# Performance work log

Measured on AMD Instinct MI355X. Metric: run time of the kernel, lower is better.

The kernel has to match this reference:

```python
import jax, jax.numpy as jnp
import numpy as np

B, N, F, C = 8, 4096, 1024, 64


def setup_inputs() -> dict:
    key = jax.random.key(0)
    k1, k2, k3 = jax.random.split(key, 3)
    x1 = jax.random.normal(k1, (B, N, F), dtype=jnp.float32)
    x2 = jax.random.normal(k2, (B, N, F), dtype=jnp.float32)
    W = jax.random.normal(k3, (C, F), dtype=jnp.float32) / np.sqrt(F)
    b = jnp.zeros((C,), dtype=jnp.float32)
    return {"x1": x1, "x2": x2, "W": W, "b": b}


def _select_max(x, W, b):
    # x: [B, N, F] -> scores [B, N, C]
    scores = jnp.einsum("bnf,cf->bnc", x, W) + b
    # per-batch, per-class index of max-scoring instance: [B, C]
    idx = jnp.argmax(scores, axis=1)
    # gather the selected instance feature vectors: [B, C, F]
    return jnp.take_along_axis(x, idx[:, :, None], axis=1)


def reference(x1, x2, W, b):
    d = _select_max(x1, W, b)
    d1 = _select_max(x2, W, b)
    return (d, d1)
```

## Files before the change

### kernel.cpp

```cpp
#include <hip/hip_runtime.h>

#define B_   8
#define N_   4096
#define F_   1024
#define C_   64
#define NBLK 16
#define MARGIN 0.08f

typedef __attribute__((ext_vector_type(8))) short bhalf8;
typedef __attribute__((ext_vector_type(4))) float f32x4;
typedef __attribute__((ext_vector_type(4))) unsigned short us4;

__device__ __forceinline__ unsigned short f2bf_rne(float x) {
    unsigned u = __builtin_bit_cast(unsigned, x);
    u += 0x7fffu + ((u >> 16) & 1u);
    return (unsigned short)(u >> 16);
}
__device__ __forceinline__ bhalf8 cvt8(float4 a, float4 b) {
    bhalf8 r;
    r[0] = (short)f2bf_rne(a.x); r[1] = (short)f2bf_rne(a.y);
    r[2] = (short)f2bf_rne(a.z); r[3] = (short)f2bf_rne(a.w);
    r[4] = (short)f2bf_rne(b.x); r[5] = (short)f2bf_rne(b.y);
    r[6] = (short)f2bf_rne(b.z); r[7] = (short)f2bf_rne(b.w);
    return r;
}

#define LEXGT(a, ai, b, bi) ((a) > (b) || ((a) == (b) && (ai) < (bi)))
#define INSERT3(vv, nn)                                                        \
    do {                                                                       \
        float _v = (vv); int _n = (nn);                                        \
        if (LEXGT(_v, _n, v0, i0)) { v2=v1; i2=i1; v1=v0; i1=i0; v0=_v; i0=_n; } \
        else if (LEXGT(_v, _n, v1, i1)) { v2=v1; i2=i1; v1=_v; i1=_n; }        \
        else if (LEXGT(_v, _n, v2, i2)) { v2=_v; i2=_n; }                      \
    } while (0)
#define INSERT4(vv, nn)                                                        \
    do {                                                                       \
        float _v = (vv); int _n = (nn);                                        \
        if (LEXGT(_v, _n, v0, i0)) { v3=v2; i3=i2; v2=v1; i2=i1; v1=v0; i1=i0; v0=_v; i0=_n; } \
        else if (LEXGT(_v, _n, v1, i1)) { v3=v2; i3=i2; v2=v1; i2=i1; v1=_v; i1=_n; } \
        else if (LEXGT(_v, _n, v2, i2)) { v3=v2; i3=i2; v2=_v; i2=_n; }        \
        else if (LEXGT(_v, _n, v3, i3)) { v3=_v; i3=_n; }                      \
    } while (0)

__global__ __launch_bounds__(256) void wconv_kernel(
    const float* __restrict__ W, unsigned short* __restrict__ Wh)
{
    int i = blockIdx.x * 256 + threadIdx.x;
    float4 v = ((const float4*)W)[i];
    us4 hh;
    hh[0] = f2bf_rne(v.x); hh[1] = f2bf_rne(v.y);
    hh[2] = f2bf_rne(v.z); hh[3] = f2bf_rne(v.w);
    ((us4*)Wh)[i] = hh;
}

__global__ __launch_bounds__(1024, 4) void score_top_kernel(
    const float* __restrict__ x1, const float* __restrict__ x2,
    const unsigned short* __restrict__ Wh,
    float* __restrict__ pv, int* __restrict__ pi)
{
    __shared__ __align__(16) char lds[131072];

    const int tid  = threadIdx.x;
    const int nb   = blockIdx.x;
    const int b    = blockIdx.y;
    const int inp  = blockIdx.z;
    const float* __restrict__ x = inp ? x2 : x1;

    const int lane = tid & 63;
    const int w    = tid >> 6;
    const int rsel = lane & 15;
    const int g    = lane >> 4;
    const int swz  = (rsel & 7) << 4;

    const int row = nb * 256 + w * 16 + rsel;
    const float* __restrict__ xr = x + ((size_t)b * N_ + row) * F_ + g * 8;

    f32x4 acc[4];
    #pragma unroll
    for (int nt = 0; nt < 4; ++nt) acc[nt] = (f32x4){0.f, 0.f, 0.f, 0.f};

    auto loadx = [&](float4* dst, int kc) {
        #pragma unroll
        for (int st = 0; st < 4; ++st) {
            dst[2 * st]     = *(const float4*)(xr + kc * 128 + st * 32);
            dst[2 * st + 1] = *(const float4*)(xr + kc * 128 + st * 32 + 4);
        }
    };
    auto compute = [&](const float4* src, int kc) {
        #pragma unroll
        for (int st = 0; st < 4; ++st) {
            bhalf8 ah = cvt8(src[2 * st], src[2 * st + 1]);
            int kb = kc * 256 + st * 64 + g * 16;
            #pragma unroll
            for (int nt = 0; nt < 4; ++nt) {
                int cls = nt * 16 + rsel;
                bhalf8 bf = *(const bhalf8*)(lds + ((cls * 2048 + kb) ^ swz));
                acc[nt] = __builtin_amdgcn_mfma_f32_16x16x32_bf16(ah, bf, acc[nt], 0, 0, 0);
            }
        }
    };

    float4 xa[8], xb[8];
    loadx(xa, 0);

    #pragma unroll
    for (int j = 0; j < 8; ++j) {
        int gi = tid + 1024 * j;
        int c = gi >> 7, kq = gi & 127;
        bhalf8 v = *(const bhalf8*)(Wh + (size_t)c * F_ + kq * 8);
        *(bhalf8*)(lds + ((c * 2048 + kq * 16) ^ ((c & 7) << 4))) = v;
    }
    __syncthreads();

    #pragma unroll
    for (int kc = 0; kc < 8; kc += 2) {
        loadx(xb, kc + 1);
        compute(xa, kc);
        if (kc + 2 < 8) loadx(xa, kc + 2);
        compute(xb, kc + 1);
    }

    float wv0[4], wv1[4], wv2[4]; int wi0[4], wi1[4], wi2[4];
    #pragma unroll
    for (int nt = 0; nt < 4; ++nt) {
        float v0 = -3.4e38f, v1 = -3.4e38f, v2 = -3.4e38f;
        int   i0 = 0x7fffffff, i1 = 0x7fffffff, i2 = 0x7fffffff;
        #pragma unroll
        for (int r = 0; r < 4; ++r) {
            int n = nb * 256 + w * 16 + 4 * g + r;
            INSERT3(acc[nt][r], n);
        }
        #pragma unroll
        for (int d = 16; d <= 32; d <<= 1) {
            float u0 = __shfl_xor(v0, d), u1 = __shfl_xor(v1, d), u2 = __shfl_xor(v2, d);
            int   j0 = __shfl_xor(i0, d), j1 = __shfl_xor(i1, d), j2 = __shfl_xor(i2, d);
            INSERT3(u0, j0); INSERT3(u1, j1); INSERT3(u2, j2);
        }
        wv0[nt] = v0; wv1[nt] = v1; wv2[nt] = v2;
        wi0[nt] = i0; wi1[nt] = i1; wi2[nt] = i2;
    }

    __syncthreads();
    float* tv = (float*)lds;
    int*   ti = (int*)(lds + 16384);
    if (lane < 16) {
        #pragma unroll
        for (int nt = 0; nt < 4; ++nt) {
            int c = nt * 16 + lane;
            tv[(w * C_ + c) * 3 + 0] = wv0[nt]; ti[(w * C_ + c) * 3 + 0] = wi0[nt];
            tv[(w * C_ + c) * 3 + 1] = wv1[nt]; ti[(w * C_ + c) * 3 + 1] = wi1[nt];
            tv[(w * C_ + c) * 3 + 2] = wv2[nt]; ti[(w * C_ + c) * 3 + 2] = wi2[nt];
        }
    }
    __syncthreads();

    if (tid < C_) {
        int c = tid;
        float v0 = -3.4e38f, v1 = -3.4e38f, v2 = -3.4e38f, v3 = -3.4e38f;
        int   i0 = 0x7fffffff, i1 = 0x7fffffff, i2 = 0x7fffffff, i3 = 0x7fffffff;
        #pragma unroll 4
        for (int ww = 0; ww < 16; ++ww)
            #pragma unroll
            for (int k = 0; k < 3; ++k)
                INSERT4(tv[(ww * C_ + c) * 3 + k], ti[(ww * C_ + c) * 3 + k]);
        int blk = ((inp * B_ + b) * NBLK + nb);
        pv[(blk * C_ + c) * 4 + 0] = v0; pi[(blk * C_ + c) * 4 + 0] = i0;
        pv[(blk * C_ + c) * 4 + 1] = v1; pi[(blk * C_ + c) * 4 + 1] = i1;
        pv[(blk * C_ + c) * 4 + 2] = v2; pi[(blk * C_ + c) * 4 + 2] = i2;
        pv[(blk * C_ + c) * 4 + 3] = v3; pi[(blk * C_ + c) * 4 + 3] = i3;
    }
}

__global__ __launch_bounds__(256) void select_gather_kernel(
    const float* __restrict__ x1, const float* __restrict__ x2,
    const float* __restrict__ W,
    const float* __restrict__ pv, const int* __restrict__ pi,
    float* __restrict__ out)
{
    const int c   = blockIdx.x;
    const int b   = blockIdx.y;
    const int inp = blockIdx.z;
    const int tid = threadIdx.x;

    __shared__ int   s_cnt;
    __shared__ float s_m;
    __shared__ int   s_cand[16];
    __shared__ float s_val[16];
    __shared__ float s_wsum[4];
    __shared__ int   s_win;

    if (tid == 0) s_cnt = 0;
    __syncthreads();

    if (tid < 64) {
        int nb = tid >> 2, k = tid & 3;
        int blk = ((inp * B_ + b) * NBLK + nb);
        int myoff = (blk * C_ + c) * 4 + k;
        float v = pv[myoff];
        float m = v;
        #pragma unroll
        for (int d = 32; d; d >>= 1) m = fmaxf(m, __shfl_xor(m, d));
        if (tid == 0) s_m = m;
        if (v >= m - MARGIN) {
            int p = atomicAdd(&s_cnt, 1);
            if (p < 16) s_cand[p] = pi[myoff];
        }
    }
    __syncthreads();

    const float* __restrict__ x = inp ? x2 : x1;
    const int ncand = min(s_cnt, 16);
    int winner;
    if (ncand == 1) {
        winner = s_cand[0];
    } else {
        for (int k = 0; k < ncand; ++k) {
            int n = s_cand[k];
            float4 xv = *(const float4*)(x + ((size_t)b * N_ + n) * F_ + tid * 4);
            float4 wq = *(const float4*)(W + (size_t)c * F_ + tid * 4);
            float p = xv.x * wq.x + xv.y * wq.y + xv.z * wq.z + xv.w * wq.w;
            #pragma unroll
            for (int d = 32; d; d >>= 1) p += __shfl_down(p, d);
            if ((tid & 63) == 0) s_wsum[tid >> 6] = p;
            __syncthreads();
            if (tid == 0) s_val[k] = s_wsum[0] + s_wsum[1] + s_wsum[2] + s_wsum[3];
            __syncthreads();
        }
        if (tid == 0) {
            float bv = s_val[0]; int bn = s_cand[0];
            for (int k = 1; k < ncand; ++k)
                if (s_val[k] > bv || (s_val[k] == bv && s_cand[k] < bn)) { bv = s_val[k]; bn = s_cand[k]; }
            s_win = bn;
        }
        __syncthreads();
        winner = s_win;
    }

    float4 vv = *(const float4*)(x + ((size_t)b * N_ + winner) * F_ + tid * 4);
    *(float4*)(out + (((size_t)inp * B_ + b) * C_ + c) * F_ + tid * 4) = vv;
}

extern "C" void kernel_launch(void* const* d_in, const int* in_sizes, int n_in,
                              void* d_out, int out_size, void* d_ws, size_t ws_size,
                              hipStream_t stream) {
    const float* x1 = (const float*)d_in[0];
    const float* x2 = (const float*)d_in[1];
    const float* W  = (const float*)d_in[2];

    unsigned short* Wh = (unsigned short*)d_ws;
    float* pv = (float*)((char*)d_ws + (size_t)C_ * F_ * sizeof(unsigned short));
    int*   pi = (int*)((char*)pv + (size_t)2 * B_ * NBLK * C_ * 4 * sizeof(float));

    wconv_kernel<<<C_ * F_ / 1024, 256, 0, stream>>>(W, Wh);
    dim3 g1(NBLK, B_, 2);
    score_top_kernel<<<g1, 1024, 0, stream>>>(x1, x2, Wh, pv, pi);
    dim3 g2(C_, B_, 2);
    select_gather_kernel<<<g2, 256, 0, stream>>>(x1, x2, W, pv, pi, (float*)d_out);
}
```

Before: 72.49 us.

## Stream x and W tiles through double-buffered LDS with direct global-to-LDS loads

Replaces the per-thread register prefetch of x plus a one-time full W copy into 128KB of LDS with a double-buffered K loop. Each step moves a 32-wide feature chunk of x and the bf16 W into swizzled LDS using global_load_lds. Blocks shrink to 64 rows and 256 threads, so the grid has 1024 blocks and LDS per block is far smaller, which should raise occupancy and overlap the streaming of x. In exchange W is reloaded once per block, every K step needs a barrier, and the candidate lists per block drop from top-4 to top-3, with select_gather adapted to 192 candidates.

```diff
diff --git a/kernel.cpp b/kernel.cpp
--- a/kernel.cpp
+++ b/kernel.cpp
@@ -4,7 +4,10 @@
 #define N_   4096
 #define F_   1024
 #define C_   64
-#define NBLK 16
+#define ROWS 64
+#define KC   32
+#define NT   (F_ / KC)
+#define NBLK (N_ / ROWS)
 #define MARGIN 0.08f
 
 typedef __attribute__((ext_vector_type(8))) short bhalf8;
@@ -24,6 +27,11 @@
     r[6] = (short)f2bf_rne(b.z); r[7] = (short)f2bf_rne(b.w);
     return r;
 }
+__device__ __forceinline__ void load_lds16(const void* g, void* l) {
+    __builtin_amdgcn_global_load_lds(
+        (const __attribute__((address_space(1))) unsigned int*)g,
+        (__attribute__((address_space(3))) unsigned int*)l, 16, 0, 0);
+}
 
 #define LEXGT(a, ai, b, bi) ((a) > (b) || ((a) == (b) && (ai) < (bi)))
 #define INSERT3(vv, nn)                                                        \
@@ -32,14 +40,6 @@
         if (LEXGT(_v, _n, v0, i0)) { v2=v1; i2=i1; v1=v0; i1=i0; v0=_v; i0=_n; } \
         else if (LEXGT(_v, _n, v1, i1)) { v2=v1; i2=i1; v1=_v; i1=_n; }        \
         else if (LEXGT(_v, _n, v2, i2)) { v2=_v; i2=_n; }                      \
-    } while (0)
-#define INSERT4(vv, nn)                                                        \
-    do {                                                                       \
-        float _v = (vv); int _n = (nn);                                        \
-        if (LEXGT(_v, _n, v0, i0)) { v3=v2; i3=i2; v2=v1; i2=i1; v1=v0; i1=i0; v0=_v; i0=_n; } \
-        else if (LEXGT(_v, _n, v1, i1)) { v3=v2; i3=i2; v2=v1; i2=i1; v1=_v; i1=_n; } \
-        else if (LEXGT(_v, _n, v2, i2)) { v3=v2; i3=i2; v2=_v; i2=_n; }        \
-        else if (LEXGT(_v, _n, v3, i3)) { v3=_v; i3=_n; }                      \
     } while (0)
 
 __global__ __launch_bounds__(256) void wconv_kernel(
@@ -53,71 +53,74 @@
     ((us4*)Wh)[i] = hh;
 }
 
-__global__ __launch_bounds__(1024, 4) void score_top_kernel(
+__global__ __launch_bounds__(256, 4) void score_top_kernel(
     const float* __restrict__ x1, const float* __restrict__ x2,
     const unsigned short* __restrict__ Wh,
     float* __restrict__ pv, int* __restrict__ pi)
 {
-    __shared__ __align__(16) char lds[131072];
+    __shared__ __align__(16) char lds[24576];
 
     const int tid  = threadIdx.x;
     const int nb   = blockIdx.x;
     const int b    = blockIdx.y;
     const int inp  = blockIdx.z;
     const float* __restrict__ x = inp ? x2 : x1;
+    const float* __restrict__ xbase = x + ((size_t)b * N_ + (size_t)nb * ROWS) * F_;
 
     const int lane = tid & 63;
     const int w    = tid >> 6;
     const int rsel = lane & 15;
     const int g    = lane >> 4;
-    const int swz  = (rsel & 7) << 4;
-
-    const int row = nb * 256 + w * 16 + rsel;
-    const float* __restrict__ xr = x + ((size_t)b * N_ + row) * F_ + g * 8;
+
+#define XOFF(buf) ((buf) * 8192)
+#define WOFF(buf) (16384 + (buf) * 4096)
+
+#define STAGE(t, buf)                                                          \
+    do {                                                                       \
+        const int f0_ = (t) * KC;                                              \
+        _Pragma("unroll")                                                      \
+        for (int j = 0; j < 2; ++j) {                                          \
+            int ii = w * 2 + j;                                                \
+            int r  = ii * 8 + (lane >> 3);                                     \
+            int cg = (lane & 7) ^ (r & 7);                                     \
+            load_lds16(xbase + (size_t)r * F_ + f0_ + cg * 4,                  \
+                       lds + XOFF(buf) + ii * 1024);                           \
+        }                                                                      \
+        {                                                                      \
+            int cls = w * 16 + (lane >> 2);                                    \
+            int cg  = (lane & 3) ^ ((cls >> 1) & 3);                           \
+            load_lds16(Wh + (size_t)cls * F_ + f0_ + cg * 8,                   \
+                       lds + WOFF(buf) + w * 1024);                            \
+        }                                                                      \
+    } while (0)
 
     f32x4 acc[4];
     #pragma unroll
     for (int nt = 0; nt < 4; ++nt) acc[nt] = (f32x4){0.f, 0.f, 0.f, 0.f};
 
-    auto loadx = [&](float4* dst, int kc) {
-        #pragma unroll
-        for (int st = 0; st < 4; ++st) {
-            dst[2 * st]     = *(const float4*)(xr + kc * 128 + st * 32);
-            dst[2 * st + 1] = *(const float4*)(xr + kc * 128 + st * 32 + 4);
-        }
-    };
-    auto compute = [&](const float4* src, int kc) {
-        #pragma unroll
-        for (int st = 0; st < 4; ++st) {
-            bhalf8 ah = cvt8(src[2 * st], src[2 * st + 1]);
-            int kb = kc * 256 + st * 64 + g * 16;
-            #pragma unroll
-            for (int nt = 0; nt < 4; ++nt) {
-                int cls = nt * 16 + rsel;
-                bhalf8 bf = *(const bhalf8*)(lds + ((cls * 2048 + kb) ^ swz));
-                acc[nt] = __builtin_amdgcn_mfma_f32_16x16x32_bf16(ah, bf, acc[nt], 0, 0, 0);
-            }
-        }
-    };
-
-    float4 xa[8], xb[8];
-    loadx(xa, 0);
-
-    #pragma unroll
-    for (int j = 0; j < 8; ++j) {
-        int gi = tid + 1024 * j;
-        int c = gi >> 7, kq = gi & 127;
-        bhalf8 v = *(const bhalf8*)(Wh + (size_t)c * F_ + kq * 8);
-        *(bhalf8*)(lds + ((c * 2048 + kq * 16) ^ ((c & 7) << 4))) = v;
-    }
-    __syncthreads();
-
-    #pragma unroll
-    for (int kc = 0; kc < 8; kc += 2) {
-        loadx(xb, kc + 1);
-        compute(xa, kc);
-        if (kc + 2 < 8) loadx(xa, kc + 2);
-        compute(xb, kc + 1);
+    const int r_    = w * 16 + rsel;
+    const int aswz0 = ((2 * g)     ^ (r_ & 7)) * 16;
+    const int aswz1 = ((2 * g + 1) ^ (r_ & 7)) * 16;
+
+    STAGE(0, 0);
+    __syncthreads();
+
+    for (int t = 0; t < NT; ++t) {
+        const int cur = t & 1;
+        if (t + 1 < NT) STAGE(t + 1, cur ^ 1);
+
+        const char* xb = lds + XOFF(cur);
+        const char* wb = lds + WOFF(cur);
+        float4 xlo = *(const float4*)(xb + r_ * 128 + aswz0);
+        float4 xhi = *(const float4*)(xb + r_ * 128 + aswz1);
+        bhalf8 ah = cvt8(xlo, xhi);
+        #pragma unroll
+        for (int nt = 0; nt < 4; ++nt) {
+            int cls = nt * 16 + rsel;
+            bhalf8 bf = *(const bhalf8*)(wb + cls * 64 + ((g ^ ((cls >> 1) & 3)) * 16));
+            acc[nt] = __builtin_amdgcn_mfma_f32_16x16x32_bf16(ah, bf, acc[nt], 0, 0, 0);
+        }
+        __syncthreads();
     }
 
     float wv0[4], wv1[4], wv2[4]; int wi0[4], wi1[4], wi2[4];
@@ -127,7 +130,7 @@
         int   i0 = 0x7fffffff, i1 = 0x7fffffff, i2 = 0x7fffffff;
         #pragma unroll
         for (int r = 0; r < 4; ++r) {
-            int n = nb * 256 + w * 16 + 4 * g + r;
+            int n = nb * ROWS + w * 16 + 4 * g + r;
             INSERT3(acc[nt][r], n);
         }
         #pragma unroll
@@ -142,7 +145,7 @@
 
     __syncthreads();
     float* tv = (float*)lds;
-    int*   ti = (int*)(lds + 16384);
+    int*   ti = (int*)(lds + 8192);
     if (lane < 16) {
         #pragma unroll
         for (int nt = 0; nt < 4; ++nt) {
@@ -156,18 +159,17 @@
 
     if (tid < C_) {
         int c = tid;
-        float v0 = -3.4e38f, v1 = -3.4e38f, v2 = -3.4e38f, v3 = -3.4e38f;
-        int   i0 = 0x7fffffff, i1 = 0x7fffffff, i2 = 0x7fffffff, i3 = 0x7fffffff;
-        #pragma unroll 4
-        for (int ww = 0; ww < 16; ++ww)
+        float v0 = -3.4e38f, v1 = -3.4e38f, v2 = -3.4e38f;
+        int   i0 = 0x7fffffff, i1 = 0x7fffffff, i2 = 0x7fffffff;
+        #pragma unroll
+        for (int ww = 0; ww < 4; ++ww)
             #pragma unroll
             for (int k = 0; k < 3; ++k)
-                INSERT4(tv[(ww * C_ + c) * 3 + k], ti[(ww * C_ + c) * 3 + k]);
+                INSERT3(tv[(ww * C_ + c) * 3 + k], ti[(ww * C_ + c) * 3 + k]);
         int blk = ((inp * B_ + b) * NBLK + nb);
-        pv[(blk * C_ + c) * 4 + 0] = v0; pi[(blk * C_ + c) * 4 + 0] = i0;
-        pv[(blk * C_ + c) * 4 + 1] = v1; pi[(blk * C_ + c) * 4 + 1] = i1;
-        pv[(blk * C_ + c) * 4 + 2] = v2; pi[(blk * C_ + c) * 4 + 2] = i2;
-        pv[(blk * C_ + c) * 4 + 3] = v3; pi[(blk * C_ + c) * 4 + 3] = i3;
+        pv[(blk * C_ + c) * 3 + 0] = v0; pi[(blk * C_ + c) * 3 + 0] = i0;
+        pv[(blk * C_ + c) * 3 + 1] = v1; pi[(blk * C_ + c) * 3 + 1] = i1;
+        pv[(blk * C_ + c) * 3 + 2] = v2; pi[(blk * C_ + c) * 3 + 2] = i2;
     }
 }
 
@@ -183,7 +185,7 @@
     const int tid = threadIdx.x;
 
     __shared__ int   s_cnt;
-    __shared__ float s_m;
+    __shared__ float s_m[4];
     __shared__ int   s_cand[16];
     __shared__ float s_val[16];
     __shared__ float s_wsum[4];
@@ -192,19 +194,24 @@
     if (tid == 0) s_cnt = 0;
     __syncthreads();
 
-    if (tid < 64) {
-        int nb = tid >> 2, k = tid & 3;
-        int blk = ((inp * B_ + b) * NBLK + nb);
-        int myoff = (blk * C_ + c) * 4 + k;
-        float v = pv[myoff];
+    float v = -3.4e38f; int id = 0;
+    if (tid < NBLK * 3) {
+        int nbk = tid / 3, k = tid - nbk * 3;
+        int blk = ((inp * B_ + b) * NBLK + nbk);
+        int off = (blk * C_ + c) * 3 + k;
+        v = pv[off]; id = pi[off];
+    }
+    {
         float m = v;
         #pragma unroll
         for (int d = 32; d; d >>= 1) m = fmaxf(m, __shfl_xor(m, d));
-        if (tid == 0) s_m = m;
-        if (v >= m - MARGIN) {
-            int p = atomicAdd(&s_cnt, 1);
-            if (p < 16) s_cand[p] = pi[myoff];
-        }
+        if ((tid & 63) == 0) s_m[tid >> 6] = m;
+    }
+    __syncthreads();
+    const float m = fmaxf(fmaxf(s_m[0], s_m[1]), fmaxf(s_m[2], s_m[3]));
+    if (v >= m - MARGIN) {
+        int p = atomicAdd(&s_cnt, 1);
+        if (p < 16) s_cand[p] = id;
     }
     __syncthreads();
 
@@ -249,11 +256,11 @@
 
     unsigned short* Wh = (unsigned short*)d_ws;
     float* pv = (float*)((char*)d_ws + (size_t)C_ * F_ * sizeof(unsigned short));
-    int*   pi = (int*)((char*)pv + (size_t)2 * B_ * NBLK * C_ * 4 * sizeof(float));
+    int*   pi = (int*)((char*)pv + (size_t)2 * B_ * NBLK * C_ * 3 * sizeof(float));
 
     wconv_kernel<<<C_ * F_ / 1024, 256, 0, stream>>>(W, Wh);
     dim3 g1(NBLK, B_, 2);
-    score_top_kernel<<<g1, 1024, 0, stream>>>(x1, x2, Wh, pv, pi);
+    score_top_kernel<<<g1, 256, 0, stream>>>(x1, x2, Wh, pv, pi);
     dim3 g2(C_, B_, 2);
     select_gather_kernel<<<g2, 256, 0, stream>>>(x1, x2, W, pv, pi, (float*)d_out);
 }
```

After: 65.98 us. -9.0%, faster.
